# Kernel tuning notes

Measured on AMD Instinct MI355X. Metric: run time of the kernel, lower is better.

## Reference

```python
import jax, jax.numpy as jnp
import numpy as np

N_NODES = 20000   # N
N_EDGES = 320000  # E (avg degree 16)
T_STEPS = 16      # T
IN_FEATS = 1      # F
HG = 64           # hidden_g
HT = 128          # hidden_t
LN_EPS = 1e-5


def _layer_norm(x, g, b):
    mu = jnp.mean(x, axis=-1, keepdims=True)
    var = jnp.mean((x - mu) ** 2, axis=-1, keepdims=True)
    return (x - mu) * jax.lax.rsqrt(var + LN_EPS) * g + b


def setup_inputs() -> dict:
    key = jax.random.key(0)
    k = jax.random.split(key, 16)
    r = lambda i, shape, s: jax.random.normal(k[i], shape, jnp.float32) * s
    return dict(
        x_seq=jax.random.normal(k[0], (1, T_STEPS, N_NODES, IN_FEATS), jnp.float32),
        edge_index=jax.random.randint(k[1], (2, N_EDGES), 0, N_NODES, dtype=jnp.int32),
        # SAGEConv layer 0: lin_l (aggregated neighbors, has bias) + lin_r (root)
        W_l0=r(2, (IN_FEATS, HG), 0.5), W_r0=r(3, (IN_FEATS, HG), 0.5), b0=jnp.zeros((HG,), jnp.float32),
        ln0_g=jnp.ones((HG,), jnp.float32), ln0_b=jnp.zeros((HG,), jnp.float32),
        # SAGEConv layer 1
        W_l1=r(4, (HG, HG), 0.1), W_r1=r(5, (HG, HG), 0.1), b1=jnp.zeros((HG,), jnp.float32),
        ln1_g=jnp.ones((HG,), jnp.float32), ln1_b=jnp.zeros((HG,), jnp.float32),
        # GRU (torch layout: gates r,z,n stacked along first dim)
        gru_Wih=r(6, (3 * HT, HG), 0.05), gru_Whh=r(7, (3 * HT, HT), 0.05),
        gru_bih=jnp.zeros((3 * HT,), jnp.float32), gru_bhh=jnp.zeros((3 * HT,), jnp.float32),
        # head
        head_W=r(8, (HT, 1), 0.05), head_b=jnp.zeros((1,), jnp.float32),
    )


def reference(x_seq, edge_index, W_l0, W_r0, b0, ln0_g, ln0_b,
              W_l1, W_r1, b1, ln1_g, ln1_b,
              gru_Wih, gru_Whh, gru_bih, gru_bhh, head_W, head_b):
    src, dst = edge_index[0], edge_index[1]
    # in-degree for mean aggregation (clamped to 1, like PyG mean aggr on isolated nodes)
    deg = jnp.clip(jax.ops.segment_sum(jnp.ones((N_EDGES,), jnp.float32), dst,
                                       num_segments=N_NODES), 1.0)[:, None]

    def sage(x, Wl, Wr, b):
        # mean over incoming neighbors, then lin_l(aggr) + lin_r(root)
        agg = jax.ops.segment_sum(x[src], dst, num_segments=N_NODES) / deg
        return agg @ Wl + x @ Wr + b

    def stack(xt):  # xt: (N, F) -> (N, HG); dropout is identity in eval mode
        h = jax.nn.relu(_layer_norm(sage(xt, W_l0, W_r0, b0), ln0_g, ln0_b))
        h = jax.nn.relu(_layer_norm(sage(h, W_l1, W_r1, b1), ln1_g, ln1_b))
        return h

    X = x_seq[0]  # (T, N, F), B == 1
    # scan over timesteps (matches the per-t Python loop, bounds peak memory)
    _, H = jax.lax.scan(lambda c, xt: (c, stack(xt)), None, X)  # H: (T, N, HG)

    def gru_step(h, xt):  # torch GRU cell; batch = N nodes
        gi = xt @ gru_Wih.T + gru_bih
        gh = h @ gru_Whh.T + gru_bhh
        ir, iz, inn = jnp.split(gi, 3, axis=-1)
        hr, hz, hn = jnp.split(gh, 3, axis=-1)
        r = jax.nn.sigmoid(ir + hr)
        z = jax.nn.sigmoid(iz + hz)
        n = jnp.tanh(inn + r * hn)
        return (1.0 - z) * n + z * h, None

    h0 = jnp.zeros((N_NODES, HT), x_seq.dtype)
    hT, _ = jax.lax.scan(gru_step, h0, H)
    y = (hT @ head_W + head_b)[:, 0]  # (N,)
    return y
```

## Files before the change

### kernel.cpp

```cpp
#include <hip/hip_runtime.h>
#include <math.h>

#define NN 20000
#define NE 320000
#define TS 16
#define HG 64
#define HTT 128
#define NG 384
#define LN_EPS 1e-5f
#define ASTR 1032

typedef __attribute__((ext_vector_type(8))) _Float16 f16x8;
typedef __attribute__((ext_vector_type(4))) _Float16 f16x4;
typedef __attribute__((ext_vector_type(2))) _Float16 f16x2;
typedef __attribute__((ext_vector_type(4))) float f32x4;

__device__ __forceinline__ float wave_sum64(float v) {
  #pragma unroll
  for (int off = 32; off > 0; off >>= 1) v += __shfl_xor(v, off, 64);
  return v;
}
__device__ __forceinline__ float quad_sum16(float v) {
  #pragma unroll
  for (int off = 1; off < 16; off <<= 1) v += __shfl_xor(v, off, 64);
  return v;
}
__device__ __forceinline__ float fast_sigmoid(float x) {
  return __builtin_amdgcn_rcpf(1.f + __expf(-x));
}
__device__ __forceinline__ float fast_tanh(float x) {
  float e = __expf(-2.f * fabsf(x));
  float th = (1.f - e) * __builtin_amdgcn_rcpf(1.f + e);
  return copysignf(th, x);
}

__global__ __launch_bounds__(256) void k_setup(
    const float* __restrict__ x_seq, float* __restrict__ xT,
    const float* __restrict__ Wih, _Float16* __restrict__ WihF,
    const float* __restrict__ Whh, _Float16* __restrict__ WhhF,
    const float* __restrict__ Wl1, const float* __restrict__ Wr1,
    _Float16* __restrict__ Wchi, _Float16* __restrict__ Wclo,
    const float* __restrict__ Wl0, const float* __restrict__ Wr0,
    const float* __restrict__ b0, const float* __restrict__ g0,
    const float* __restrict__ be0, float* __restrict__ P,
    int* __restrict__ cnt) {
  int gid = blockIdx.x * 256 + threadIdx.x;
  int stride = gridDim.x * 256;
  for (int i = gid; i < NN * TS; i += stride) {
    int t = i / NN, n = i - t * NN;
    xT[n * 16 + t] = x_seq[i];
  }
  for (int i = gid; i < NG * HG; i += stride) WihF[i] = (_Float16)Wih[i];
  for (int i = gid; i < NG * HTT; i += stride) WhhF[i] = (_Float16)Whh[i];
  for (int i = gid; i < HG * 128; i += stride) {
    int n = i >> 7, k = i & 127;
    float x = (k < HG) ? Wl1[k * HG + n] : Wr1[(k - HG) * HG + n];
    _Float16 h = (_Float16)x;
    Wchi[i] = h;
    Wclo[i] = (_Float16)(x - (float)h);
  }
  for (int i = gid; i < NN; i += stride) cnt[i] = 0;
  if (blockIdx.x == 0 && threadIdx.x < 64) {
    int f = threadIdx.x;
    float u = Wl0[f], v = Wr0[f], c = b0[f], g = g0[f];
    float um = wave_sum64(u) * (1.f / 64.f);
    float vm = wave_sum64(v) * (1.f / 64.f);
    float cm = wave_sum64(c) * (1.f / 64.f);
    float uc = u - um, vc = v - vm, cc = c - cm;
    float muu = wave_sum64(uc * uc) * (1.f / 64.f);
    float mvv = wave_sum64(vc * vc) * (1.f / 64.f);
    float mcc = wave_sum64(cc * cc) * (1.f / 64.f);
    float muv = wave_sum64(uc * vc) * (1.f / 64.f);
    float muc = wave_sum64(uc * cc) * (1.f / 64.f);
    float mvc = wave_sum64(vc * cc) * (1.f / 64.f);
    P[f] = uc * g; P[64 + f] = vc * g; P[128 + f] = cc * g; P[192 + f] = be0[f];
    if (f == 0) {
      P[256] = muu; P[257] = mvv; P[258] = mcc;
      P[259] = muv; P[260] = muc; P[261] = mvc;
    }
  }
}

__global__ void k_hist(const int* __restrict__ dst, int* cnt) {
  int e = blockIdx.x * blockDim.x + threadIdx.x;
  if (e < NE) atomicAdd(&cnt[dst[e]], 1);
}

__global__ void k_scan(int* cnt, int* row_ptr, float* deg_inv) {
  __shared__ int s[1024];
  const int PER = 20;
  int tid = threadIdx.x;
  int base = tid * PER;
  int vloc[PER], dloc[PER];
  int sum = 0;
  #pragma unroll
  for (int j = 0; j < PER; j++) {
    int n = base + j;
    int d = (n < NN) ? cnt[n] : 0;
    vloc[j] = sum;
    dloc[j] = d;
    sum += d;
  }
  s[tid] = sum;
  __syncthreads();
  for (int off = 1; off < 1024; off <<= 1) {
    int t = (tid >= off) ? s[tid - off] : 0;
    __syncthreads();
    s[tid] += t;
    __syncthreads();
  }
  int excl = s[tid] - sum;
  #pragma unroll
  for (int j = 0; j < PER; j++) {
    int n = base + j;
    if (n < NN) {
      int rp = excl + vloc[j];
      row_ptr[n] = rp;
      cnt[n] = rp;
      int d = dloc[j];
      deg_inv[n] = 1.0f / (float)((d > 1) ? d : 1);
    }
  }
  if (tid == 1023) row_ptr[NN] = s[1023];
}

__global__ void k_fill(const int* __restrict__ src, const int* __restrict__ dst,
                       int* cursor, int* col) {
  int e = blockIdx.x * blockDim.x + threadIdx.x;
  if (e < NE) {
    int p = atomicAdd(&cursor[dst[e]], 1);
    col[p] = src[e];
  }
}

__global__ __launch_bounds__(256) void k_h0_fused(
    const float* __restrict__ xT,
    const int* __restrict__ row_ptr, const int* __restrict__ col,
    const float* __restrict__ deg_inv,
    const float* __restrict__ P,
    _Float16* __restrict__ h0r,
    _Float16* __restrict__ code) {
  int lane = threadIdx.x & 63;
  int n = blockIdx.x * 4 + (threadIdx.x >> 6);
  int grp = lane >> 4, tl = lane & 15;
  int beg = row_ptr[n];
  int deg = row_ptr[n + 1] - beg;
  float s0 = 0.f, s1 = 0.f;
  int iters = (deg + 7) >> 3;
  for (int it = 0; it < iters; it++) {
    int e0 = it * 8 + grp, e1 = it * 8 + 4 + grp;
    bool v0 = e0 < deg, v1 = e1 < deg;
    int i0 = v0 ? e0 : 0, i1 = v1 ? e1 : 0;
    int c0 = col[beg + i0];
    int c1 = col[beg + i1];
    float x0 = xT[c0 * 16 + tl];
    float x1 = xT[c1 * 16 + tl];
    s0 += v0 ? x0 : 0.f;
    s1 += v1 ? x1 : 0.f;
  }
  float s = s0 + s1;
  s += __shfl_xor(s, 16, 64);
  s += __shfl_xor(s, 32, 64);
  float aggv = s * deg_inv[n];
  float xv = xT[n * 16 + tl];
  float muu = P[256], mvv = P[257], mcc = P[258];
  float muv = P[259], muc = P[260], mvc = P[261];
  if (lane < 16) {
    float a = aggv, x = xv;
    float var = a * a * muu + x * x * mvv + mcc
              + 2.f * (a * x * muv + a * muc + x * mvc);
    float rstd = rsqrtf(var + LN_EPS);
    f16x4 cw;
    cw[0] = (_Float16)(a * rstd);
    cw[1] = (_Float16)(x * rstd);
    cw[2] = (_Float16)rstd;
    cw[3] = (_Float16)0.f;
    *(f16x4*)&code[(size_t)n * 64 + (lane & 7) * 8 + (lane >> 3) * 4] = cw;
  }
  #pragma unroll
  for (int half = 0; half < 2; half++) {
    int c = lane + half * 64;
    int t = c >> 3, f8 = (c & 7) * 8;
    float a = __shfl(aggv, t, 64);
    float x = __shfl(xv, t, 64);
    float var = a * a * muu + x * x * mvv + mcc
              + 2.f * (a * x * muv + a * muc + x * mvc);
    float rstd = rsqrtf(var + LN_EPS);
    f16x8 o;
    #pragma unroll
    for (int j = 0; j < 8; j++) {
      int f = f8 + j;
      float d = a * P[f] + x * P[64 + f] + P[128 + f];
      o[j] = (_Float16)fmaxf(d * rstd + P[192 + f], 0.f);
    }
    *(f16x8*)&h0r[(size_t)n * 1024 + c * 8] = o;
  }
}

__global__ __launch_bounds__(256) void k_sage_fused(
    const _Float16* __restrict__ h0r,
    const int* __restrict__ row_ptr, const int* __restrict__ col,
    const _Float16* __restrict__ code,
    const float* __restrict__ P,
    const _Float16* __restrict__ Wchi, const _Float16* __restrict__ Wclo,
    const float* __restrict__ b1, const float* __restrict__ g1, const float* __restrict__ be1,
    _Float16* __restrict__ Ht_all) {
  __shared__ _Float16 aggL[16 * ASTR];
  int tid = threadIdx.x;
  int lane = tid & 63, wave = tid >> 6;
  int col16 = lane & 15, quad = lane >> 4;
  int m0 = blockIdx.x * 16;

  {
    const f16x2 h2z = {(_Float16)0.f, (_Float16)0.f};
    const f16x2 h2o = {(_Float16)1.f, (_Float16)1.f};
    int f1 = (lane & 7) * 8;
    f16x2 Pu2[4], Pv2[4], Pc2[4], Pb2[4];
    #pragma unroll
    for (int j = 0; j < 4; j++) {
      Pu2[j] = (f16x2){(_Float16)P[f1 + 2*j],       (_Float16)P[f1 + 2*j + 1]};
      Pv2[j] = (f16x2){(_Float16)P[64 + f1 + 2*j],  (_Float16)P[64 + f1 + 2*j + 1]};
      Pc2[j] = (f16x2){(_Float16)P[128 + f1 + 2*j], (_Float16)P[128 + f1 + 2*j + 1]};
      Pb2[j] = (f16x2){(_Float16)P[192 + f1 + 2*j], (_Float16)P[192 + f1 + 2*j + 1]};
    }
    int codeoff = (lane >> 3) * 8;

    int i4 = lane >> 4;
    int slot = lane & 15;
    int ni = m0 + wave * 4 + i4;
    int beg_i = row_ptr[ni];
    int d_i = row_ptr[ni + 1] - beg_i;
    int cv0 = (slot < d_i) ? col[beg_i + slot] : 0;
    int cv1 = (slot + 16 < d_i) ? col[beg_i + 16 + slot] : 0;

    auto ldcode = [&](int c) -> f16x8 {
      return *(const f16x8*)(code + (size_t)c * 64 + codeoff);
    };

#define ACCUM(cd, mk, A1, A2)                                              \
  { f16x2 _A1 = {cd[0], cd[0]}, _X1 = {cd[1], cd[1]}, _C1 = {cd[2], cd[2]};\
    f16x2 _A2 = {cd[4], cd[4]}, _X2 = {cd[5], cd[5]}, _C2 = {cd[6], cd[6]};\
    _Pragma("unroll")                                                      \
    for (int j = 0; j < 4; j++) {                                          \
      f16x2 d1 = __builtin_elementwise_fma(_A1, Pu2[j],                    \
                  __builtin_elementwise_fma(_X1, Pv2[j],                   \
                   __builtin_elementwise_fma(_C1, Pc2[j], Pb2[j])));       \
      d1 = __builtin_elementwise_max(d1, h2z);                             \
      A1[j] = __builtin_elementwise_fma(d1, mk, A1[j]);                    \
      f16x2 d2 = __builtin_elementwise_fma(_A2, Pu2[j],                    \
                  __builtin_elementwise_fma(_X2, Pv2[j],                   \
                   __builtin_elementwise_fma(_C2, Pc2[j], Pb2[j])));       \
      d2 = __builtin_elementwise_max(d2, h2z);                             \
      A2[j] = __builtin_elementwise_fma(d2, mk, A2[j]);                    \
    } }

#define BLOCK8(CV, EB, DREL, FULL)                                         \
  { f16x8 cds[8];                                                          \
    _Pragma("unroll")                                                      \
    for (int e = 0; e < 8; e++)                                            \
      cds[e] = ldcode(__builtin_amdgcn_readlane(CV, ib + (EB) + e));       \
    _Pragma("unroll")                                                      \
    for (int e = 0; e < 8; e++) {                                          \
      f16x2 mk = (FULL) ? h2o : ((((EB) + e) < (DREL)) ? h2o : h2z);       \
      if (e & 1) ACCUM(cds[e], mk, aO1, aO2)                               \
      else       ACCUM(cds[e], mk, aE1, aE2)                               \
    } }

    for (int i = 0; i < 4; i++) {
      int ib = i << 4;
      int deg = __builtin_amdgcn_readlane(d_i, ib);
      int bg  = __builtin_amdgcn_readlane(beg_i, ib);
      f16x2 aE1[4], aO1[4], aE2[4], aO2[4];
      #pragma unroll
      for (int j = 0; j < 4; j++) {
        aE1[j] = h2z; aO1[j] = h2z; aE2[j] = h2z; aO2[j] = h2z;
      }
      if (deg >= 16) {
        BLOCK8(cv0, 0, 16, true)
        BLOCK8(cv0, 8, 16, true)
      } else {
        BLOCK8(cv0, 0, deg, false)
        BLOCK8(cv0, 8, deg, false)
      }
      if (deg > 16) {
        int dr = deg - 16;
        if (deg >= 32) {
          BLOCK8(cv1, 0, 16, true)
          BLOCK8(cv1, 8, 16, true)
        } else {
          BLOCK8(cv1, 0, dr, false)
          BLOCK8(cv1, 8, dr, false)
        }
        for (int e3 = 32; e3 < deg; e3++) {
          f16x8 cdt = ldcode(col[bg + e3]);
          ACCUM(cdt, h2o, aE1, aE2)
        }
      }
      float dif = 1.0f / (float)((deg > 1) ? deg : 1);
      _Float16 dih = (_Float16)dif;
      f16x2 di2 = {dih, dih};
      union { f16x8 v; f16x2 h[4]; } u0, u1;
      #pragma unroll
      for (int j = 0; j < 4; j++) {
        u0.h[j] = (aE1[j] + aO1[j]) * di2;
        u1.h[j] = (aE2[j] + aO2[j]) * di2;
      }
      int nl = wave * 4 + i;
      *(f16x8*)&aggL[nl * ASTR + lane * 8] = u0.v;
      *(f16x8*)&aggL[nl * ASTR + 512 + lane * 8] = u1.v;
    }
#undef BLOCK8
#undef ACCUM
  }
  __syncthreads();

  for (int ts = 0; ts < 4; ts++) {
    int t = wave * 4 + ts;
    f32x4 acc[4];
    #pragma unroll
    for (int nt = 0; nt < 4; nt++) acc[nt] = (f32x4){0.f, 0.f, 0.f, 0.f};

    #pragma unroll
    for (int kk = 0; kk < 2; kk++) {
      f16x8 ah = *(const f16x8*)&aggL[col16 * ASTR + t * 64 + kk * 32 + quad * 8];
      #pragma unroll
      for (int nt = 0; nt < 4; nt++) {
        int nf = nt * 16 + col16;
        f16x8 bh = *(const f16x8*)&Wchi[nf * 128 + kk * 32 + quad * 8];
        f16x8 bl = *(const f16x8*)&Wclo[nf * 128 + kk * 32 + quad * 8];
        acc[nt] = __builtin_amdgcn_mfma_f32_16x16x32_f16(ah, bh, acc[nt], 0, 0, 0);
        acc[nt] = __builtin_amdgcn_mfma_f32_16x16x32_f16(ah, bl, acc[nt], 0, 0, 0);
      }
    }
    #pragma unroll
    for (int kk = 0; kk < 2; kk++) {
      f16x8 ah = *(const f16x8*)&h0r[(size_t)(m0 + col16) * 1024 + t * 64 + kk * 32 + quad * 8];
      #pragma unroll
      for (int nt = 0; nt < 4; nt++) {
        int nf = nt * 16 + col16;
        f16x8 bh = *(const f16x8*)&Wchi[nf * 128 + 64 + kk * 32 + quad * 8];
        f16x8 bl = *(const f16x8*)&Wclo[nf * 128 + 64 + kk * 32 + quad * 8];
        acc[nt] = __builtin_amdgcn_mfma_f32_16x16x32_f16(ah, bh, acc[nt], 0, 0, 0);
        acc[nt] = __builtin_amdgcn_mfma_f32_16x16x32_f16(ah, bl, acc[nt], 0, 0, 0);
      }
    }

    float bias[4], gg[4], bb[4];
    #pragma unroll
    for (int nt = 0; nt < 4; nt++) {
      int nf = nt * 16 + col16;
      bias[nt] = b1[nf]; gg[nt] = g1[nf]; bb[nt] = be1[nf];
    }
    #pragma unroll
    for (int r = 0; r < 4; r++) {
      float v[4];
      #pragma unroll
      for (int nt = 0; nt < 4; nt++) v[nt] = acc[nt][r] + bias[nt];
      float s = (v[0] + v[1]) + (v[2] + v[3]);
      float mu = quad_sum16(s) * (1.f / 64.f);
      float sq = 0.f;
      #pragma unroll
      for (int nt = 0; nt < 4; nt++) { v[nt] -= mu; sq += v[nt] * v[nt]; }
      float var = quad_sum16(sq) * (1.f / 64.f);
      float rstd = rsqrtf(var + LN_EPS);
      int m = m0 + quad * 4 + r;
      size_t base = ((size_t)t * NN + m) * HG;
      #pragma unroll
      for (int nt = 0; nt < 4; nt++) {
        float o = fmaxf(v[nt] * rstd * gg[nt] + bb[nt], 0.f);
        Ht_all[base + nt * 16 + col16] = (_Float16)o;
      }
    }
  }
}

__global__ __launch_bounds__(256, 2) void k_gru_all(
    const _Float16* __restrict__ Ht_all,
    const _Float16* __restrict__ WihF,
    const _Float16* __restrict__ WhhF,
    const float* __restrict__ bih, const float* __restrict__ bhh,
    const float* __restrict__ headW, const float* __restrict__ headb,
    float* __restrict__ out) {
  __shared__ _Float16 WihL[NG * 64];
  __shared__ _Float16 hL[2][32 * 128];
  __shared__ float yL[4][32];

  int tid = threadIdx.x;
  int lane = tid & 63, wave = tid >> 6;
  int col16 = lane & 15, quad = lane >> 4;
  int m0 = blockIdx.x * 32;
  int gb = 2 * wave;

  for (int i = tid; i < NG * 8; i += 256) {
    int g = i >> 3, k8 = i & 7;
    *(f16x8*)&WihL[g * 64 + ((k8 + g) & 7) * 8] = *(const f16x8*)&WihF[g * 64 + k8 * 8];
  }
  for (int i = tid; i < 2 * 32 * 128; i += 256) hL[0][i] = (_Float16)0.f;

  int gts[6];
  #pragma unroll
  for (int t6 = 0; t6 < 6; t6++)
    gts[t6] = (t6 < 2) ? (gb + t6) : (t6 < 4) ? (8 + gb + t6 - 2) : (16 + gb + t6 - 4);

  f16x8 wgh[4][6];
  #pragma unroll
  for (int kk = 0; kk < 4; kk++)
    #pragma unroll
    for (int t6 = 0; t6 < 6; t6++)
      wgh[kk][t6] = *(const f16x8*)&WhhF[(size_t)(gts[t6] * 16 + col16) * HTT + kk * 32 + quad * 8];

  int jj[2]; float bR[2], bZ[2], bNi[2], bNh[2], hw[2];
  int waddr[2][4][2];
  #pragma unroll
  for (int js = 0; js < 2; js++) {
    int j = (gb + js) * 16 + col16;
    jj[js] = j;
    bR[js]  = bih[j] + bhh[j];
    bZ[js]  = bih[HTT + j] + bhh[HTT + j];
    bNi[js] = bih[2 * HTT + j];
    bNh[js] = bhh[2 * HTT + j];
    hw[js]  = headW[j];
    #pragma unroll
    for (int mt = 0; mt < 2; mt++)
      #pragma unroll
      for (int r = 0; r < 4; r++) {
        int row = mt * 16 + quad * 4 + r;
        waddr[mt][r][js] = row * 128 + (((j >> 3) + row) & 15) * 8 + (j & 7);
      }
  }
  float hreg[2][4][2];
  #pragma unroll
  for (int mt = 0; mt < 2; mt++)
    #pragma unroll
    for (int r = 0; r < 4; r++) { hreg[mt][r][0] = 0.f; hreg[mt][r][1] = 0.f; }

  size_t aoff[2][2];
  #pragma unroll
  for (int kk = 0; kk < 2; kk++)
    #pragma unroll
    for (int mt = 0; mt < 2; mt++)
      aoff[kk][mt] = (size_t)(m0 + mt * 16 + col16) * HG + kk * 32 + quad * 8;

  __syncthreads();

  for (int t = 0; t < TS; t++) {
    const _Float16* hcur = hL[t & 1];
    _Float16* hnxt = hL[(t + 1) & 1];

    f32x4 acc[8][2];
    #pragma unroll
    for (int a = 0; a < 8; a++) {
      acc[a][0] = (f32x4){0.f, 0.f, 0.f, 0.f};
      acc[a][1] = (f32x4){0.f, 0.f, 0.f, 0.f};
    }

    const _Float16* AH = Ht_all + (size_t)t * NN * HG;
    f16x8 gah[2][2];
    #pragma unroll
    for (int kk = 0; kk < 2; kk++)
      #pragma unroll
      for (int mt = 0; mt < 2; mt++)
        gah[kk][mt] = *(const f16x8*)&AH[aoff[kk][mt]];

    #pragma unroll
    for (int kk = 0; kk < 4; kk++) {
      f16x8 ah[2];
      #pragma unroll
      for (int mt = 0; mt < 2; mt++) {
        int row = mt * 16 + col16;
        int k8 = kk * 4 + quad;
        ah[mt] = *(const f16x8*)&hcur[row * 128 + ((k8 + row) & 15) * 8];
      }
      #pragma unroll
      for (int t6 = 0; t6 < 6; t6++) {
        int ai = (t6 < 4) ? t6 : t6 + 2;
        #pragma unroll
        for (int mt = 0; mt < 2; mt++)
          acc[ai][mt] = __builtin_amdgcn_mfma_f32_16x16x32_f16(ah[mt], wgh[kk][t6], acc[ai][mt], 0, 0, 0);
      }
    }
    #pragma unroll
    for (int kk = 0; kk < 2; kk++) {
      #pragma unroll
      for (int t6 = 0; t6 < 6; t6++) {
        int g = gts[t6] * 16 + col16;
        int k8 = kk * 4 + quad;
        f16x8 b = *(const f16x8*)&WihL[g * 64 + ((k8 + g) & 7) * 8];
        #pragma unroll
        for (int mt = 0; mt < 2; mt++)
          acc[t6][mt] = __builtin_amdgcn_mfma_f32_16x16x32_f16(gah[kk][mt], b, acc[t6][mt], 0, 0, 0);
      }
    }

    #pragma unroll
    for (int mt = 0; mt < 2; mt++) {
      #pragma unroll
      for (int r = 0; r < 4; r++) {
        #pragma unroll
        for (int js = 0; js < 2; js++) {
          float R  = acc[0 + js][mt][r] + bR[js];
          float Z  = acc[2 + js][mt][r] + bZ[js];
          float Ni = acc[4 + js][mt][r] + bNi[js];
          float Nh = acc[6 + js][mt][r] + bNh[js];
          float rg = fast_sigmoid(R);
          float zg = fast_sigmoid(Z);
          float nn = fast_tanh(Ni + rg * Nh);
          float hn = nn + zg * (hreg[mt][r][js] - nn);
          hreg[mt][r][js] = hn;
          hnxt[waddr[mt][r][js]] = (_Float16)hn;
        }
      }
    }
    __syncthreads();
  }

  #pragma unroll
  for (int mt = 0; mt < 2; mt++) {
    #pragma unroll
    for (int r = 0; r < 4; r++) {
      float py = hreg[mt][r][0] * hw[0] + hreg[mt][r][1] * hw[1];
      py = quad_sum16(py);
      if (col16 == 0) yL[wave][mt * 16 + quad * 4 + r] = py;
    }
  }
  __syncthreads();
  if (tid < 32)
    out[m0 + tid] = yL[0][tid] + yL[1][tid] + yL[2][tid] + yL[3][tid] + headb[0];
}

extern "C" void kernel_launch(void* const* d_in, const int* in_sizes, int n_in,
                              void* d_out, int out_size, void* d_ws, size_t ws_size,
                              hipStream_t stream) {
  const float* x_seq = (const float*)d_in[0];
  const int*   edge  = (const int*)d_in[1];
  const float* Wl0   = (const float*)d_in[2];
  const float* Wr0   = (const float*)d_in[3];
  const float* b0    = (const float*)d_in[4];
  const float* g0    = (const float*)d_in[5];
  const float* be0   = (const float*)d_in[6];
  const float* Wl1   = (const float*)d_in[7];
  const float* Wr1   = (const float*)d_in[8];
  const float* b1    = (const float*)d_in[9];
  const float* g1    = (const float*)d_in[10];
  const float* be1   = (const float*)d_in[11];
  const float* Wih   = (const float*)d_in[12];
  const float* Whh   = (const float*)d_in[13];
  const float* bih   = (const float*)d_in[14];
  const float* bhh   = (const float*)d_in[15];
  const float* headW = (const float*)d_in[16];
  const float* headb = (const float*)d_in[17];
  float* out = (float*)d_out;

  const int* srcp = edge;
  const int* dstp = edge + NE;

  char* ws = (char*)d_ws;
  size_t off = 0;
  auto alloc = [&](size_t bytes) -> void* {
    void* p = ws + off;
    off += (bytes + 255) & ~(size_t)255;
    return p;
  };
  int*   cnt     = (int*)alloc(NN * 4);
  int*   row_ptr = (int*)alloc((NN + 1) * 4);
  int*   col     = (int*)alloc(NE * 4);
  float* deg_inv = (float*)alloc(NN * 4);
  float* xT      = (float*)alloc((size_t)NN * TS * 4);
  float* P       = (float*)alloc(512 * 4);
  _Float16* h0r  = (_Float16*)alloc((size_t)NN * 1024 * 2);
  _Float16* code = (_Float16*)alloc((size_t)NN * 64 * 2);
  _Float16* Ht_all = (_Float16*)alloc((size_t)TS * NN * HG * 2);
  _Float16* WihF = (_Float16*)alloc((size_t)NG * HG * 2);
  _Float16* WhhF = (_Float16*)alloc((size_t)NG * HTT * 2);
  _Float16* Wchi = (_Float16*)alloc((size_t)HG * 128 * 2);
  _Float16* Wclo = (_Float16*)alloc((size_t)HG * 128 * 2);
  (void)ws_size; (void)in_sizes; (void)n_in; (void)out_size;

  k_setup<<<1250, 256, 0, stream>>>(x_seq, xT, Wih, WihF, Whh, WhhF,
                                    Wl1, Wr1, Wchi, Wclo,
                                    Wl0, Wr0, b0, g0, be0, P, cnt);
  k_hist<<<(NE + 255) / 256, 256, 0, stream>>>(dstp, cnt);
  k_scan<<<1, 1024, 0, stream>>>(cnt, row_ptr, deg_inv);
  k_fill<<<(NE + 255) / 256, 256, 0, stream>>>(srcp, dstp, cnt, col);
  k_h0_fused<<<NN / 4, 256, 0, stream>>>(xT, row_ptr, col, deg_inv, P, h0r, code);
  k_sage_fused<<<NN / 16, 256, 0, stream>>>(h0r, row_ptr, col, code, P,
                                            Wchi, Wclo, b1, g1, be1, Ht_all);
  k_gru_all<<<NN / 32, 256, 0, stream>>>(Ht_all, WihF, WhhF, bih, bhh,
                                         headW, headb, out);
}
```

Baseline: 366.8 us.

## Split fused SAGE layer-1 kernel into separate gather and GEMM kernels

The fused layer-1 kernel, which gathered neighbour codes into shared memory and then ran MFMA GEMMs, is split into two kernels. k_gather handles one node per wave and reads a pre-duplicated code layout (code2, twice the size) so the half2 broadcast shuffles go away. It writes the aggregated fp16 features to a new global buffer, and k_gemm then reads them back. This drops the 33KB shared-memory tile and may raise occupancy and load balance. In exchange it adds about 40MB of extra global write and read traffic plus one more launch.

```diff
diff --git a/kernel.cpp b/kernel.cpp
--- a/kernel.cpp
+++ b/kernel.cpp
@@ -8,7 +8,6 @@
 #define HTT 128
 #define NG 384
 #define LN_EPS 1e-5f
-#define ASTR 1032
 
 typedef __attribute__((ext_vector_type(8))) _Float16 f16x8;
 typedef __attribute__((ext_vector_type(4))) _Float16 f16x4;
@@ -139,7 +138,7 @@
     const float* __restrict__ deg_inv,
     const float* __restrict__ P,
     _Float16* __restrict__ h0r,
-    _Float16* __restrict__ code) {
+    _Float16* __restrict__ code2) {
   int lane = threadIdx.x & 63;
   int n = blockIdx.x * 4 + (threadIdx.x >> 6);
   int grp = lane >> 4, tl = lane & 15;
@@ -170,12 +169,11 @@
     float var = a * a * muu + x * x * mvv + mcc
               + 2.f * (a * x * muv + a * muc + x * mvc);
     float rstd = rsqrtf(var + LN_EPS);
-    f16x4 cw;
-    cw[0] = (_Float16)(a * rstd);
-    cw[1] = (_Float16)(x * rstd);
-    cw[2] = (_Float16)rstd;
-    cw[3] = (_Float16)0.f;
-    *(f16x4*)&code[(size_t)n * 64 + (lane & 7) * 8 + (lane >> 3) * 4] = cw;
+    _Float16 Ah = (_Float16)(a * rstd);
+    _Float16 Xh = (_Float16)(x * rstd);
+    _Float16 Ch = (_Float16)rstd;
+    f16x8 cw = {Ah, Ah, Xh, Xh, Ch, Ch, (_Float16)0.f, (_Float16)0.f};
+    *(f16x8*)&code2[(size_t)n * 128 + (lane & 7) * 16 + (lane >> 3) * 8] = cw;
   }
   #pragma unroll
   for (int half = 0; half < 2; half++) {
@@ -197,122 +195,114 @@
   }
 }
 
-__global__ __launch_bounds__(256) void k_sage_fused(
+__global__ __launch_bounds__(256) void k_gather(
+    const int* __restrict__ row_ptr, const int* __restrict__ col,
+    const _Float16* __restrict__ code2,
+    const float* __restrict__ P,
+    _Float16* __restrict__ agg) {
+  int lane = threadIdx.x & 63;
+  int n = blockIdx.x * 4 + (threadIdx.x >> 6);
+  const f16x2 h2z = {(_Float16)0.f, (_Float16)0.f};
+  const f16x2 h2o = {(_Float16)1.f, (_Float16)1.f};
+  int f1 = (lane & 7) * 8;
+  int tmod = lane >> 3;
+  f16x2 Pu2[4], Pv2[4], Pc2[4], Pb2[4];
+  #pragma unroll
+  for (int j = 0; j < 4; j++) {
+    Pu2[j] = (f16x2){(_Float16)P[f1 + 2*j],       (_Float16)P[f1 + 2*j + 1]};
+    Pv2[j] = (f16x2){(_Float16)P[64 + f1 + 2*j],  (_Float16)P[64 + f1 + 2*j + 1]};
+    Pc2[j] = (f16x2){(_Float16)P[128 + f1 + 2*j], (_Float16)P[128 + f1 + 2*j + 1]};
+    Pb2[j] = (f16x2){(_Float16)P[192 + f1 + 2*j], (_Float16)P[192 + f1 + 2*j + 1]};
+  }
+  int beg = row_ptr[n];
+  int deg = row_ptr[n + 1] - beg;
+  int cvAll = (lane < deg) ? col[beg + lane] : 0;
+
+  f16x2 aE1[4], aO1[4], aE2[4], aO2[4];
+  #pragma unroll
+  for (int j = 0; j < 4; j++) { aE1[j] = h2z; aO1[j] = h2z; aE2[j] = h2z; aO2[j] = h2z; }
+
+#define ACC_SET(c, mk, FULL, ACC)                                          \
+  { f16x2 _A = __builtin_shufflevector(c, c, 0, 1);                        \
+    f16x2 _X = __builtin_shufflevector(c, c, 2, 3);                        \
+    f16x2 _C = __builtin_shufflevector(c, c, 4, 5);                        \
+    _Pragma("unroll")                                                      \
+    for (int j = 0; j < 4; j++) {                                          \
+      f16x2 d = __builtin_elementwise_fma(_A, Pu2[j],                      \
+                 __builtin_elementwise_fma(_X, Pv2[j],                     \
+                  __builtin_elementwise_fma(_C, Pc2[j], Pb2[j])));         \
+      d = __builtin_elementwise_max(d, h2z);                               \
+      ACC[j] = (FULL) ? (ACC[j] + d)                                       \
+                      : __builtin_elementwise_fma(d, mk, ACC[j]);          \
+    } }
+
+  int nb4 = (deg + 3) >> 2;
+  if (nb4 > 16) nb4 = 16;
+  for (int b = 0; b < nb4; b++) {
+    int eb = b << 2;
+    f16x8 cA[4], cB[4];
+    #pragma unroll
+    for (int e = 0; e < 4; e++) {
+      int c = __builtin_amdgcn_readlane(cvAll, eb + e);
+      const _Float16* cp = code2 + (size_t)c * 128 + tmod * 16;
+      cA[e] = *(const f16x8*)cp;
+      cB[e] = *(const f16x8*)(cp + 8);
+    }
+    if (eb + 4 <= deg) {
+      #pragma unroll
+      for (int e = 0; e < 4; e++) {
+        if (e & 1) { ACC_SET(cA[e], h2o, true, aO1) ACC_SET(cB[e], h2o, true, aO2) }
+        else       { ACC_SET(cA[e], h2o, true, aE1) ACC_SET(cB[e], h2o, true, aE2) }
+      }
+    } else {
+      #pragma unroll
+      for (int e = 0; e < 4; e++) {
+        f16x2 mk = ((eb + e) < deg) ? h2o : h2z;
+        if (e & 1) { ACC_SET(cA[e], mk, false, aO1) ACC_SET(cB[e], mk, false, aO2) }
+        else       { ACC_SET(cA[e], mk, false, aE1) ACC_SET(cB[e], mk, false, aE2) }
+      }
+    }
+  }
+  for (int e = 64; e < deg; e++) {
+    int c = col[beg + e];
+    const _Float16* cp = code2 + (size_t)c * 128 + tmod * 16;
+    f16x8 ca = *(const f16x8*)cp;
+    f16x8 cb = *(const f16x8*)(cp + 8);
+    ACC_SET(ca, h2o, true, aE1) ACC_SET(cb, h2o, true, aE2)
+  }
+#undef ACC_SET
+
+  float dif = 1.0f / (float)((deg > 1) ? deg : 1);
+  _Float16 dih = (_Float16)dif;
+  f16x2 di2 = {dih, dih};
+  union { f16x8 v; f16x2 h[4]; } u0, u1;
+  #pragma unroll
+  for (int j = 0; j < 4; j++) {
+    u0.h[j] = (aE1[j] + aO1[j]) * di2;
+    u1.h[j] = (aE2[j] + aO2[j]) * di2;
+  }
+  *(f16x8*)&agg[(size_t)n * 1024 + lane * 8] = u0.v;
+  *(f16x8*)&agg[(size_t)n * 1024 + 512 + lane * 8] = u1.v;
+}
+
+__global__ __launch_bounds__(256) void k_gemm(
     const _Float16* __restrict__ h0r,
-    const int* __restrict__ row_ptr, const int* __restrict__ col,
-    const _Float16* __restrict__ code,
-    const float* __restrict__ P,
+    const _Float16* __restrict__ agg,
     const _Float16* __restrict__ Wchi, const _Float16* __restrict__ Wclo,
     const float* __restrict__ b1, const float* __restrict__ g1, const float* __restrict__ be1,
     _Float16* __restrict__ Ht_all) {
-  __shared__ _Float16 aggL[16 * ASTR];
   int tid = threadIdx.x;
   int lane = tid & 63, wave = tid >> 6;
   int col16 = lane & 15, quad = lane >> 4;
   int m0 = blockIdx.x * 16;
 
-  {
-    const f16x2 h2z = {(_Float16)0.f, (_Float16)0.f};
-    const f16x2 h2o = {(_Float16)1.f, (_Float16)1.f};
-    int f1 = (lane & 7) * 8;
-    f16x2 Pu2[4], Pv2[4], Pc2[4], Pb2[4];
-    #pragma unroll
-    for (int j = 0; j < 4; j++) {
-      Pu2[j] = (f16x2){(_Float16)P[f1 + 2*j],       (_Float16)P[f1 + 2*j + 1]};
-      Pv2[j] = (f16x2){(_Float16)P[64 + f1 + 2*j],  (_Float16)P[64 + f1 + 2*j + 1]};
-      Pc2[j] = (f16x2){(_Float16)P[128 + f1 + 2*j], (_Float16)P[128 + f1 + 2*j + 1]};
-      Pb2[j] = (f16x2){(_Float16)P[192 + f1 + 2*j], (_Float16)P[192 + f1 + 2*j + 1]};
-    }
-    int codeoff = (lane >> 3) * 8;
-
-    int i4 = lane >> 4;
-    int slot = lane & 15;
-    int ni = m0 + wave * 4 + i4;
-    int beg_i = row_ptr[ni];
-    int d_i = row_ptr[ni + 1] - beg_i;
-    int cv0 = (slot < d_i) ? col[beg_i + slot] : 0;
-    int cv1 = (slot + 16 < d_i) ? col[beg_i + 16 + slot] : 0;
-
-    auto ldcode = [&](int c) -> f16x8 {
-      return *(const f16x8*)(code + (size_t)c * 64 + codeoff);
-    };
-
-#define ACCUM(cd, mk, A1, A2)                                              \
-  { f16x2 _A1 = {cd[0], cd[0]}, _X1 = {cd[1], cd[1]}, _C1 = {cd[2], cd[2]};\
-    f16x2 _A2 = {cd[4], cd[4]}, _X2 = {cd[5], cd[5]}, _C2 = {cd[6], cd[6]};\
-    _Pragma("unroll")                                                      \
-    for (int j = 0; j < 4; j++) {                                          \
-      f16x2 d1 = __builtin_elementwise_fma(_A1, Pu2[j],                    \
-                  __builtin_elementwise_fma(_X1, Pv2[j],                   \
-                   __builtin_elementwise_fma(_C1, Pc2[j], Pb2[j])));       \
-      d1 = __builtin_elementwise_max(d1, h2z);                             \
-      A1[j] = __builtin_elementwise_fma(d1, mk, A1[j]);                    \
-      f16x2 d2 = __builtin_elementwise_fma(_A2, Pu2[j],                    \
-                  __builtin_elementwise_fma(_X2, Pv2[j],                   \
-                   __builtin_elementwise_fma(_C2, Pc2[j], Pb2[j])));       \
-      d2 = __builtin_elementwise_max(d2, h2z);                             \
-      A2[j] = __builtin_elementwise_fma(d2, mk, A2[j]);                    \
-    } }
-
-#define BLOCK8(CV, EB, DREL, FULL)                                         \
-  { f16x8 cds[8];                                                          \
-    _Pragma("unroll")                                                      \
-    for (int e = 0; e < 8; e++)                                            \
-      cds[e] = ldcode(__builtin_amdgcn_readlane(CV, ib + (EB) + e));       \
-    _Pragma("unroll")                                                      \
-    for (int e = 0; e < 8; e++) {                                          \
-      f16x2 mk = (FULL) ? h2o : ((((EB) + e) < (DREL)) ? h2o : h2z);       \
-      if (e & 1) ACCUM(cds[e], mk, aO1, aO2)                               \
-      else       ACCUM(cds[e], mk, aE1, aE2)                               \
-    } }
-
-    for (int i = 0; i < 4; i++) {
-      int ib = i << 4;
-      int deg = __builtin_amdgcn_readlane(d_i, ib);
-      int bg  = __builtin_amdgcn_readlane(beg_i, ib);
-      f16x2 aE1[4], aO1[4], aE2[4], aO2[4];
-      #pragma unroll
-      for (int j = 0; j < 4; j++) {
-        aE1[j] = h2z; aO1[j] = h2z; aE2[j] = h2z; aO2[j] = h2z;
-      }
-      if (deg >= 16) {
-        BLOCK8(cv0, 0, 16, true)
-        BLOCK8(cv0, 8, 16, true)
-      } else {
-        BLOCK8(cv0, 0, deg, false)
-        BLOCK8(cv0, 8, deg, false)
-      }
-      if (deg > 16) {
-        int dr = deg - 16;
-        if (deg >= 32) {
-          BLOCK8(cv1, 0, 16, true)
-          BLOCK8(cv1, 8, 16, true)
-        } else {
-          BLOCK8(cv1, 0, dr, false)
-          BLOCK8(cv1, 8, dr, false)
-        }
-        for (int e3 = 32; e3 < deg; e3++) {
-          f16x8 cdt = ldcode(col[bg + e3]);
-          ACCUM(cdt, h2o, aE1, aE2)
-        }
-      }
-      float dif = 1.0f / (float)((deg > 1) ? deg : 1);
-      _Float16 dih = (_Float16)dif;
-      f16x2 di2 = {dih, dih};
-      union { f16x8 v; f16x2 h[4]; } u0, u1;
-      #pragma unroll
-      for (int j = 0; j < 4; j++) {
-        u0.h[j] = (aE1[j] + aO1[j]) * di2;
-        u1.h[j] = (aE2[j] + aO2[j]) * di2;
-      }
-      int nl = wave * 4 + i;
-      *(f16x8*)&aggL[nl * ASTR + lane * 8] = u0.v;
-      *(f16x8*)&aggL[nl * ASTR + 512 + lane * 8] = u1.v;
-    }
-#undef BLOCK8
-#undef ACCUM
-  }
-  __syncthreads();
+  float bias[4], gg[4], bb[4];
+  #pragma unroll
+  for (int nt = 0; nt < 4; nt++) {
+    int nf = nt * 16 + col16;
+    bias[nt] = b1[nf]; gg[nt] = g1[nf]; bb[nt] = be1[nf];
+  }
+  size_t rowbase = (size_t)(m0 + col16) * 1024;
 
   for (int ts = 0; ts < 4; ts++) {
     int t = wave * 4 + ts;
@@ -320,37 +310,35 @@
     #pragma unroll
     for (int nt = 0; nt < 4; nt++) acc[nt] = (f32x4){0.f, 0.f, 0.f, 0.f};
 
+    f16x8 aa[2], ar[2];
     #pragma unroll
     for (int kk = 0; kk < 2; kk++) {
-      f16x8 ah = *(const f16x8*)&aggL[col16 * ASTR + t * 64 + kk * 32 + quad * 8];
+      aa[kk] = *(const f16x8*)&agg[rowbase + t * 64 + kk * 32 + quad * 8];
+      ar[kk] = *(const f16x8*)&h0r[rowbase + t * 64 + kk * 32 + quad * 8];
+    }
+    #pragma unroll
+    for (int kk = 0; kk < 2; kk++) {
       #pragma unroll
       for (int nt = 0; nt < 4; nt++) {
         int nf = nt * 16 + col16;
         f16x8 bh = *(const f16x8*)&Wchi[nf * 128 + kk * 32 + quad * 8];
         f16x8 bl = *(const f16x8*)&Wclo[nf * 128 + kk * 32 + quad * 8];
-        acc[nt] = __builtin_amdgcn_mfma_f32_16x16x32_f16(ah, bh, acc[nt], 0, 0, 0);
-        acc[nt] = __builtin_amdgcn_mfma_f32_16x16x32_f16(ah, bl, acc[nt], 0, 0, 0);
+        acc[nt] = __builtin_amdgcn_mfma_f32_16x16x32_f16(aa[kk], bh, acc[nt], 0, 0, 0);
+        acc[nt] = __builtin_amdgcn_mfma_f32_16x16x32_f16(aa[kk], bl, acc[nt], 0, 0, 0);
       }
     }
     #pragma unroll
     for (int kk = 0; kk < 2; kk++) {
-      f16x8 ah = *(const f16x8*)&h0r[(size_t)(m0 + col16) * 1024 + t * 64 + kk * 32 + quad * 8];
       #pragma unroll
       for (int nt = 0; nt < 4; nt++) {
         int nf = nt * 16 + col16;
         f16x8 bh = *(const f16x8*)&Wchi[nf * 128 + 64 + kk * 32 + quad * 8];
         f16x8 bl = *(const f16x8*)&Wclo[nf * 128 + 64 + kk * 32 + quad * 8];
-        acc[nt] = __builtin_amdgcn_mfma_f32_16x16x32_f16(ah, bh, acc[nt], 0, 0, 0);
-        acc[nt] = __builtin_amdgcn_mfma_f32_16x16x32_f16(ah, bl, acc[nt], 0, 0, 0);
-      }
-    }
-
-    float bias[4], gg[4], bb[4];
-    #pragma unroll
-    for (int nt = 0; nt < 4; nt++) {
-      int nf = nt * 16 + col16;
-      bias[nt] = b1[nf]; gg[nt] = g1[nf]; bb[nt] = be1[nf];
-    }
+        acc[nt] = __builtin_amdgcn_mfma_f32_16x16x32_f16(ar[kk], bh, acc[nt], 0, 0, 0);
+        acc[nt] = __builtin_amdgcn_mfma_f32_16x16x32_f16(ar[kk], bl, acc[nt], 0, 0, 0);
+      }
+    }
+
     #pragma unroll
     for (int r = 0; r < 4; r++) {
       float v[4];
@@ -568,7 +556,8 @@
   float* xT      = (float*)alloc((size_t)NN * TS * 4);
   float* P       = (float*)alloc(512 * 4);
   _Float16* h0r  = (_Float16*)alloc((size_t)NN * 1024 * 2);
-  _Float16* code = (_Float16*)alloc((size_t)NN * 64 * 2);
+  _Float16* code2= (_Float16*)alloc((size_t)NN * 128 * 2);
+  _Float16* agg  = (_Float16*)alloc((size_t)NN * 1024 * 2);
   _Float16* Ht_all = (_Float16*)alloc((size_t)TS * NN * HG * 2);
   _Float16* WihF = (_Float16*)alloc((size_t)NG * HG * 2);
   _Float16* WhhF = (_Float16*)alloc((size_t)NG * HTT * 2);
@@ -582,9 +571,9 @@
   k_hist<<<(NE + 255) / 256, 256, 0, stream>>>(dstp, cnt);
   k_scan<<<1, 1024, 0, stream>>>(cnt, row_ptr, deg_inv);
   k_fill<<<(NE + 255) / 256, 256, 0, stream>>>(srcp, dstp, cnt, col);
-  k_h0_fused<<<NN / 4, 256, 0, stream>>>(xT, row_ptr, col, deg_inv, P, h0r, code);
-  k_sage_fused<<<NN / 16, 256, 0, stream>>>(h0r, row_ptr, col, code, P,
-                                            Wchi, Wclo, b1, g1, be1, Ht_all);
+  k_h0_fused<<<NN / 4, 256, 0, stream>>>(xT, row_ptr, col, deg_inv, P, h0r, code2);
+  k_gather<<<NN / 4, 256, 0, stream>>>(row_ptr, col, code2, P, agg);
+  k_gemm<<<NN / 16, 256, 0, stream>>>(h0r, agg, Wchi, Wclo, b1, g1, be1, Ht_all);
   k_gru_all<<<NN / 32, 256, 0, stream>>>(Ht_all, WihF, WhhF, bih, bhh,
                                          headW, headb, out);
 }
```

Measured after the change: 364.8 us. Within noise of the previous version (-0.6%).
